# Optimization experiments

Hardware: AMD Instinct MI355X
Metric: run time of the kernel (lower is better)

The kernel has to match this reference:

```python
import jax, jax.numpy as jnp
import numpy as np
from jax import lax

EPS = 1e-5
S_CENTROIDS = 2048
K_NEIGH = 32


def _fps(xyz, S):
    """Farthest point sampling. xyz: (B,N,3) -> idx (B,S) int32."""
    B, N, _ = xyz.shape

    def body(carry, _):
        dist, farthest = carry  # (B,N), (B,)
        centroid = jnp.take_along_axis(xyz, farthest[:, None, None], axis=1)  # (B,1,3)
        d = jnp.sum((xyz - centroid) ** 2, axis=-1)  # (B,N)
        dist = jnp.minimum(dist, d)
        nxt = jnp.argmax(dist, axis=-1).astype(jnp.int32)
        return (dist, nxt), farthest

    init = (jnp.full((B, N), 1e10, xyz.dtype), jnp.zeros((B,), jnp.int32))
    _, idx = lax.scan(body, init, None, length=S)
    return idx.T  # (B,S)


def _knn(q, p, K):
    """q: (B,S,3) queries, p: (B,N,3) points -> idx (B,S,K) of K nearest."""
    d = (jnp.sum(q * q, -1)[:, :, None] + jnp.sum(p * p, -1)[:, None, :]
         - 2.0 * jnp.einsum('bsd,bnd->bsn', q, p))  # (B,S,N) sq dists
    _, idx = lax.top_k(-d, K)
    return idx


def _mlp_layer(x, w, g, b, m, v):
    # x: (B,S,K,Cin); 1x1 conv == channel matmul, then eval-mode BN, then ReLU
    x = jnp.einsum('bskc,oc->bsko', x, w)
    x = (x - m) * (g * lax.rsqrt(v + EPS)) + b
    return jax.nn.relu(x)


def setup_inputs() -> dict:
    key = jax.random.key(0)
    ks = jax.random.split(key, 8)
    B, N, D = 4, 8192, 64
    inp = {
        'xyz': jax.random.normal(ks[0], (B, N, 3), jnp.float32),
        'points': jax.random.normal(ks[1], (B, D, N), jnp.float32),
        'w0': jax.random.normal(ks[2], (64, 67), jnp.float32) * (1.0 / np.sqrt(67)),
        'g0': jnp.ones((64,), jnp.float32), 'b0': jnp.zeros((64,), jnp.float32),
        'm0': jnp.zeros((64,), jnp.float32), 'v0': jnp.ones((64,), jnp.float32),
        'w1': jax.random.normal(ks[3], (64, 64), jnp.float32) * (1.0 / np.sqrt(64)),
        'g1': jnp.ones((64,), jnp.float32), 'b1': jnp.zeros((64,), jnp.float32),
        'm1': jnp.zeros((64,), jnp.float32), 'v1': jnp.ones((64,), jnp.float32),
        'w2': jax.random.normal(ks[4], (128, 64), jnp.float32) * (1.0 / np.sqrt(64)),
        'g2': jnp.ones((128,), jnp.float32), 'b2': jnp.zeros((128,), jnp.float32),
        'm2': jnp.zeros((128,), jnp.float32), 'v2': jnp.ones((128,), jnp.float32),
    }
    return inp


def reference(xyz, points, w0, g0, b0, m0, v0, w1, g1, b1, m1, v1,
              w2, g2, b2, m2, v2):
    B, N, _ = xyz.shape
    S, K = S_CENTROIDS, K_NEIGH

    # FPS centroids (S < N path of the module)
    fps_idx = _fps(xyz, S)                                        # (B,S)
    new_xyz = jnp.take_along_axis(xyz, fps_idx[..., None], axis=1)  # (B,S,3)

    # KNN grouping
    idx = _knn(new_xyz, xyz, K)                                   # (B,S,K)
    grouped_xyz = jnp.take_along_axis(xyz[:, None], idx[..., None], axis=2)  # (B,S,K,3)
    grouped_xyz = grouped_xyz - new_xyz[:, :, None, :]

    # gather neighbor features: points (B,D,N) -> (B,N,D) -> (B,S,K,D)
    pts = jnp.transpose(points, (0, 2, 1))
    neigh = jnp.take_along_axis(pts[:, None], idx[..., None], axis=2)
    grouped = jnp.concatenate([grouped_xyz, neigh], axis=-1)      # (B,S,K,3+D)

    x = _mlp_layer(grouped, w0, g0, b0, m0, v0)
    x = _mlp_layer(x, w1, g1, b1, m1, v1)
    x = _mlp_layer(x, w2, g2, b2, m2, v2)                         # (B,S,K,128)

    new_points = jnp.transpose(jnp.max(x, axis=2), (0, 2, 1))     # (B,128,S)
    return new_xyz, new_points
```

## Files before the change

kernel.cpp:

```cpp
#include <hip/hip_runtime.h>
#include <cfloat>
#include <climits>

#define NPTS   8192
#define SCENT  2048
#define KNEIGH 32
#define BATCH  4
#define DFEAT  64
#define FPS_T  512
#define PPT    16
#define NW     8
#define CAP    64

#define DPPMAX(u, ctrl, rmask)                                                        \
    { unsigned _t = (unsigned)__builtin_amdgcn_update_dpp(0, (int)(u), (ctrl),        \
                                                          (rmask), 0xf, false);      \
      (u) = ((u) > _t) ? (u) : _t; }

__global__ __launch_bounds__(FPS_T, 1) void fps_kernel(const float* __restrict__ xyz,
                                                       float* __restrict__ new_xyz) {
    const int b = blockIdx.x, t = threadIdx.x;
    const int lane = t & 63, w = t >> 6;
    const float* X = xyz + (size_t)b * NPTS * 3;

    __shared__ float sx[NPTS], sy[NPTS], sz[NPTS];
    __shared__ float hx[SCENT], hy[SCENT], hz[SCENT];
    __shared__ uint2 slots[2][NW];
    __shared__ int   scand[CAP];
    __shared__ int   scnt;
    __shared__ double sdd[2][NW];
    __shared__ double sfv[NW];
    __shared__ int   sfo[NW];

    for (int p = t; p < NPTS; p += FPS_T) {
        sx[p] = X[3 * p + 0]; sy[p] = X[3 * p + 1]; sz[p] = X[3 * p + 2];
    }

    float px[PPT], py[PPT], pz[PPT], dist[PPT];
#pragma unroll
    for (int j = 0; j < PPT; ++j) {
        int p = t + FPS_T * j;
        px[j] = X[3 * p + 0]; py[j] = X[3 * p + 1]; pz[j] = X[3 * p + 2];
        dist[j] = 1e10f;
    }
    float cx = X[0], cy = X[1], cz = X[2];
    int buf = 0;
    __syncthreads();

#pragma unroll 1
    for (int s = 0; s < SCENT; ++s) {
        if (t == 0) { hx[s] = cx; hy[s] = cy; hz[s] = cz; }

        float ma = -1.f, mb = -1.f; int ia = 0, ib = 0;
#pragma unroll
        for (int j = 0; j < PPT; j += 2) {
            {
                float dx = px[j] - cx, dy = py[j] - cy, dz = pz[j] - cz;
                float d  = fmaf(dx, dx, fmaf(dy, dy, dz * dz));
                float nd = fminf(dist[j], d); dist[j] = nd;
                bool g = nd > ma; ma = g ? nd : ma; ia = g ? (t + FPS_T * j) : ia;
            }
            {
                float dx = px[j+1] - cx, dy = py[j+1] - cy, dz = pz[j+1] - cz;
                float d  = fmaf(dx, dx, fmaf(dy, dy, dz * dz));
                float nd = fminf(dist[j+1], d); dist[j+1] = nd;
                bool g = nd > mb; mb = g ? nd : mb; ib = g ? (t + FPS_T * (j+1)) : ib;
            }
        }
        bool gb = mb > ma;
        float m = gb ? mb : ma;
        int  mi = gb ? ib : ia;

        unsigned myU = __float_as_uint(m);
        unsigned u = myU;
        DPPMAX(u, 0x111, 0xf);
        DPPMAX(u, 0x112, 0xf);
        DPPMAX(u, 0x114, 0xf);
        DPPMAX(u, 0x118, 0xf);
        DPPMAX(u, 0x142, 0xa);
        DPPMAX(u, 0x143, 0xc);
        const unsigned wu = (unsigned)__builtin_amdgcn_readlane((int)u, 63);

        unsigned long long wb = __ballot(myU == wu);
        const int wl   = __ffsll(wb) - 1;
        const int widx = __builtin_amdgcn_readlane(mi, wl);
        const float thwf = __fmul_rn(__uint_as_float(wu), 0.999998f);
        int cnt = 0;
#pragma unroll
        for (int j = 0; j < PPT; ++j) cnt += (dist[j] >= thwf) ? 1 : 0;
        unsigned long long c1 = __ballot(cnt >= 1);
        unsigned long long c2 = __ballot(cnt >= 2);
        const unsigned tw = (c2 || __popcll(c1) >= 2) ? 1u : 0u;
        if (lane == 0)
            slots[buf][w] = make_uint2(wu, (unsigned)widx | (tw << 14));
        __syncthreads();

        uint2 sv[NW];
#pragma unroll
        for (int k = 0; k < NW; ++k) sv[k] = slots[buf][k];
        unsigned gu = sv[0].x;
#pragma unroll
        for (int k = 1; k < NW; ++k) gu = (sv[k].x > gu) ? sv[k].x : gu;
        const float gvf = __uint_as_float(gu);
        const float gthf = __fmul_rn(gvf, 0.999998f);
        const unsigned ugth = __float_as_uint(gthf);
        int nw = 0;
#pragma unroll
        for (int k = 0; k < NW; ++k) nw += (sv[k].x >= ugth) ? 1 : 0;
        unsigned meta = 0;
#pragma unroll
        for (int k = NW - 1; k >= 0; --k) if (sv[k].x == gu) meta = sv[k].y;
        const int wtie = (meta >> 14) & 1;
        int i1 = (int)(meta & 0x3fffu);

        if (nw >= 2 || wtie) {
            if (t == 0) scnt = 0;
            __syncthreads();
#pragma unroll
            for (int j = 0; j < PPT; ++j) {
                if (dist[j] >= gthf) {
                    int slot = atomicAdd(&scnt, 1);
                    if (slot < CAP) scand[slot] = t + FPS_T * j;
                }
            }
            __syncthreads();
            const int mm = scnt;
            if (mm <= CAP) {
                double bd = -1.0; int bi = INT_MAX;
#pragma unroll 1
                for (int k = 0; k < mm; ++k) {
                    const int pos = scand[k];
                    const double pxd = (double)sx[pos], pyd = (double)sy[pos],
                                 pzd = (double)sz[pos];
                    double dd = 1e10;
                    for (int i = t; i <= s; i += FPS_T) {
                        double ddx = __dsub_rn(pxd, (double)hx[i]);
                        double ddy = __dsub_rn(pyd, (double)hy[i]);
                        double ddz = __dsub_rn(pzd, (double)hz[i]);
                        double d = __dadd_rn(__dadd_rn(__dmul_rn(ddx, ddx), __dmul_rn(ddy, ddy)),
                                             __dmul_rn(ddz, ddz));
                        dd = fmin(dd, d);
                    }
#pragma unroll
                    for (int off = 32; off >= 1; off >>= 1)
                        dd = fmin(dd, __shfl_down(dd, off));
                    if (lane == 0) sdd[k & 1][w] = dd;
                    __syncthreads();
                    double ddm = sdd[k & 1][0];
#pragma unroll
                    for (int w2 = 1; w2 < NW; ++w2) ddm = fmin(ddm, sdd[k & 1][w2]);
                    if (ddm > bd || (ddm == bd && pos < bi)) { bd = ddm; bi = pos; }
                }
                i1 = bi;
            } else {
                double bv = -1.0; int bi = INT_MAX;
#pragma unroll 1
                for (int j = 0; j < PPT; ++j) {
                    const double pxd = (double)px[j], pyd = (double)py[j], pzd = (double)pz[j];
                    double dd = 1e10;
                    for (int i = 0; i <= s; ++i) {
                        double ddx = __dsub_rn(pxd, (double)hx[i]);
                        double ddy = __dsub_rn(pyd, (double)hy[i]);
                        double ddz = __dsub_rn(pzd, (double)hz[i]);
                        double d = __dadd_rn(__dadd_rn(__dmul_rn(ddx, ddx), __dmul_rn(ddy, ddy)),
                                             __dmul_rn(ddz, ddz));
                        dd = fmin(dd, d);
                    }
                    int pidx = t + FPS_T * j;
                    if (dd > bv || (dd == bv && pidx < bi)) { bv = dd; bi = pidx; }
                }
#pragma unroll
                for (int off = 32; off >= 1; off >>= 1) {
                    double ov = __shfl_down(bv, off);
                    int    oi = __shfl_down(bi, off);
                    if (ov > bv || (ov == bv && oi < bi)) { bv = ov; bi = oi; }
                }
                if (lane == 0) { sfv[w] = bv; sfo[w] = bi; }
                __syncthreads();
                bv = sfv[0]; bi = sfo[0];
#pragma unroll
                for (int w2 = 1; w2 < NW; ++w2) {
                    double ov = sfv[w2]; int oi = sfo[w2];
                    if (ov > bv || (ov == bv && oi < bi)) { bv = ov; bi = oi; }
                }
                i1 = bi;
            }
            __syncthreads();
        }
        cx = sx[i1]; cy = sy[i1]; cz = sz[i1];
        buf ^= 1;
    }
    __syncthreads();
    for (int i = t; i < SCENT; i += FPS_T) {
        float* o = new_xyz + (size_t)(b * SCENT + i) * 3;
        o[0] = hx[i]; o[1] = hy[i]; o[2] = hz[i];
    }
}

__global__ void transpose_kernel(const float* __restrict__ pts, float* __restrict__ out) {
    __shared__ float tile[32][33];
    const int b  = blockIdx.z;
    const int n0 = blockIdx.x * 32, d0 = blockIdx.y * 32;
    const int tx = threadIdx.x, ty = threadIdx.y;
#pragma unroll
    for (int i = 0; i < 4; ++i)
        tile[ty + 8 * i][tx] =
            pts[(size_t)b * DFEAT * NPTS + (size_t)(d0 + ty + 8 * i) * NPTS + n0 + tx];
    __syncthreads();
#pragma unroll
    for (int i = 0; i < 4; ++i)
        out[(size_t)b * NPTS * DFEAT + (size_t)(n0 + ty + 8 * i) * DFEAT + d0 + tx] =
            tile[tx][ty + 8 * i];
}

__global__ __launch_bounds__(256) void knn_kernel(const float* __restrict__ xyz,
                                                  const float* __restrict__ new_xyz,
                                                  int* __restrict__ knn_idx) {
    const int b    = blockIdx.y;
    const int wid  = threadIdx.x >> 6;
    const int lane = threadIdx.x & 63;
    const int qi   = blockIdx.x * 4 + wid;

    __shared__ float4 sp[2048];
    __shared__ double sp2[2048];

    const float* q = new_xyz + (size_t)(b * SCENT + qi) * 3;
    const double qx = (double)q[0], qy = (double)q[1], qz = (double)q[2];
    const double q2 = __dadd_rn(__dadd_rn(__dmul_rn(qx, qx), __dmul_rn(qy, qy)),
                                __dmul_rn(qz, qz));

    double ld   = DBL_MAX;
    int    li   = 0x7fffffff;
    double taud = DBL_MAX;
    int    taui = 0x7fffffff;

    const float* Xb = xyz + (size_t)b * NPTS * 3;
#pragma unroll 1
    for (int c = 0; c < 4; ++c) {
        __syncthreads();
#pragma unroll
        for (int r = 0; r < 8; ++r) {
            int pl = r * 256 + threadIdx.x;
            int p  = c * 2048 + pl;
            float x = Xb[3 * p + 0], y = Xb[3 * p + 1], z = Xb[3 * p + 2];
            sp[pl] = make_float4(x, y, z, 0.0f);
            double dx = (double)x, dy = (double)y, dz = (double)z;
            sp2[pl] = __dadd_rn(__dadd_rn(__dmul_rn(dx, dx), __dmul_rn(dy, dy)),
                                __dmul_rn(dz, dz));
        }
        __syncthreads();
#pragma unroll 1
        for (int i = 0; i < 32; ++i) {
            const int pl   = i * 64 + lane;
            const int pidx = c * 2048 + pl;
            float4 P = sp[pl];
            double px = (double)P.x, py = (double)P.y, pz = (double)P.z;
            double qp = __dadd_rn(__dadd_rn(__dmul_rn(qx, px), __dmul_rn(qy, py)),
                                  __dmul_rn(qz, pz));
            double d  = __dsub_rn(__dadd_rn(q2, sp2[pl]), __dmul_rn(2.0, qp));
            bool cand = (d < taud) || (d == taud && pidx < taui);
            unsigned long long m = __ballot(cand);
            while (m) {
                int sl = __ffsll((unsigned long long)m) - 1;
                m &= m - 1;
                double dv = __shfl(d, sl);
                int    iv = __shfl(pidx, sl);
                if (dv < taud || (dv == taud && iv < taui)) {
                    bool gt = (lane < 32) && (ld > dv || (ld == dv && li > iv));
                    unsigned long long gm = __ballot(gt);
                    double ud = __shfl_up(ld, 1);
                    int    ui = __shfl_up(li, 1);
                    if (gt) { ld = ud; li = ui; }
                    bool first = gt && ((lane == 0) || !((gm >> (lane - 1)) & 1ull));
                    if (first) { ld = dv; li = iv; }
                    taud = __shfl(ld, 31);
                    taui = __shfl(li, 31);
                }
            }
        }
    }
    if (lane < 32) knn_idx[(size_t)(b * SCENT + qi) * KNEIGH + lane] = li;
}

__global__ __launch_bounds__(256) void mlp_kernel(
    const float* __restrict__ xyz, const float* __restrict__ new_xyz,
    const float* __restrict__ ptsT, const int* __restrict__ knn_idx,
    const float* __restrict__ w0, const float* __restrict__ g0,
    const float* __restrict__ b0, const float* __restrict__ m0,
    const float* __restrict__ v0, const float* __restrict__ w1,
    const float* __restrict__ g1, const float* __restrict__ b1,
    const float* __restrict__ m1, const float* __restrict__ v1,
    const float* __restrict__ w2, const float* __restrict__ g2,
    const float* __restrict__ b2, const float* __restrict__ m2,
    const float* __restrict__ v2, float* __restrict__ out_points) {

    __shared__ float regA[8192];
    __shared__ float regB[4096];
    __shared__ float prm[512];

    const int t = threadIdx.x;
    if (t < 64) {
        float a0v = g0[t] / sqrtf(v0[t] + 1e-5f);
        prm[t]       = a0v;
        prm[64 + t]  = b0[t] - m0[t] * a0v;
        float a1v = g1[t] / sqrtf(v1[t] + 1e-5f);
        prm[128 + t] = a1v;
        prm[192 + t] = b1[t] - m1[t] * a1v;
    } else if (t < 192) {
        int o = t - 64;
        float a2v = g2[o] / sqrtf(v2[o] + 1e-5f);
        prm[256 + o] = a2v;
        prm[384 + o] = b2[o] - m2[o] * a2v;
    }
    for (int idx = t; idx < 64 * 68; idx += 256) {
        int o = idx / 68, i = idx - o * 68;
        float v;
        if (i < 64)      v = w0[o * 67 + 3 + i];
        else if (i < 67) v = w0[o * 67 + (i - 64)];
        else             v = 0.0f;
        regA[idx] = v;
    }
    for (int idx = t; idx < 64 * 64; idx += 256) regB[idx] = w1[idx];
    __syncthreads();

    const int gid = blockIdx.x * 256 + t;
    const int sl  = gid >> 5;
    const int s   = sl & (SCENT - 1);
    const int b   = sl >> 11;
    const int nidx = knn_idx[gid];

    const float* q  = new_xyz + (size_t)(b * SCENT + s) * 3;
    const float* P3 = xyz + (size_t)(b * NPTS + nidx) * 3;
    const float dx = P3[0] - q[0], dy = P3[1] - q[1], dz = P3[2] - q[2];

    const float4* F = (const float4*)(ptsT + ((size_t)b * NPTS + nidx) * 64);
    float4 xv[17];
#pragma unroll
    for (int i = 0; i < 16; ++i) xv[i] = F[i];
    xv[16] = make_float4(dx, dy, dz, 0.0f);

    float h0[64];
    const float4* W0 = (const float4*)regA;
#pragma unroll
    for (int o = 0; o < 64; ++o) {
        float acc = 0.f;
#pragma unroll
        for (int i = 0; i < 17; ++i) {
            float4 w = W0[o * 17 + i];
            acc = fmaf(xv[i].x, w.x, acc);
            acc = fmaf(xv[i].y, w.y, acc);
            acc = fmaf(xv[i].z, w.z, acc);
            acc = fmaf(xv[i].w, w.w, acc);
        }
        h0[o] = fmaxf(fmaf(acc, prm[o], prm[64 + o]), 0.f);
    }
    __syncthreads();
    for (int idx = t; idx < 128 * 64; idx += 256) regA[idx] = w2[idx];
    __syncthreads();

    float h1[64];
    const float4* W1 = (const float4*)regB;
#pragma unroll
    for (int o = 0; o < 64; ++o) {
        float acc = 0.f;
#pragma unroll
        for (int i = 0; i < 16; ++i) {
            float4 w = W1[o * 16 + i];
            acc = fmaf(h0[4 * i + 0], w.x, acc);
            acc = fmaf(h0[4 * i + 1], w.y, acc);
            acc = fmaf(h0[4 * i + 2], w.z, acc);
            acc = fmaf(h0[4 * i + 3], w.w, acc);
        }
        h1[o] = fmaxf(fmaf(acc, prm[128 + o], prm[192 + o]), 0.f);
    }

    const float4* W2 = (const float4*)regA;
    float* outp = out_points + (size_t)b * 128 * SCENT + s;
    const int lane = t & 63;
#pragma unroll 1
    for (int o = 0; o < 128; ++o) {
        float acc = 0.f;
#pragma unroll
        for (int i = 0; i < 16; ++i) {
            float4 w = W2[o * 16 + i];
            acc = fmaf(h1[4 * i + 0], w.x, acc);
            acc = fmaf(h1[4 * i + 1], w.y, acc);
            acc = fmaf(h1[4 * i + 2], w.z, acc);
            acc = fmaf(h1[4 * i + 3], w.w, acc);
        }
        float y = fmaxf(fmaf(acc, prm[256 + o], prm[384 + o]), 0.f);
#pragma unroll
        for (int off = 16; off >= 1; off >>= 1) y = fmaxf(y, __shfl_xor(y, off));
        if ((lane & 31) == 0) outp[(size_t)o * SCENT] = y;
    }
}

extern "C" void kernel_launch(void* const* d_in, const int* in_sizes, int n_in,
                              void* d_out, int out_size, void* d_ws, size_t ws_size,
                              hipStream_t stream) {
    const float* xyz    = (const float*)d_in[0];
    const float* points = (const float*)d_in[1];
    const float* w0 = (const float*)d_in[2];
    const float* g0 = (const float*)d_in[3];
    const float* b0 = (const float*)d_in[4];
    const float* m0 = (const float*)d_in[5];
    const float* v0 = (const float*)d_in[6];
    const float* w1 = (const float*)d_in[7];
    const float* g1 = (const float*)d_in[8];
    const float* b1 = (const float*)d_in[9];
    const float* m1 = (const float*)d_in[10];
    const float* v1 = (const float*)d_in[11];
    const float* w2 = (const float*)d_in[12];
    const float* g2 = (const float*)d_in[13];
    const float* b2 = (const float*)d_in[14];
    const float* m2 = (const float*)d_in[15];
    const float* v2 = (const float*)d_in[16];

    float* out_xyz    = (float*)d_out;
    float* out_points = (float*)d_out + (size_t)BATCH * SCENT * 3;

    char* ws = (char*)d_ws;
    int*   knn_idx = (int*)(ws + 32768);
    float* ptsT    = (float*)(ws + 32768 + (size_t)BATCH * SCENT * KNEIGH * 4);

    fps_kernel<<<BATCH, FPS_T, 0, stream>>>(xyz, out_xyz);
    transpose_kernel<<<dim3(NPTS / 32, DFEAT / 32, BATCH), dim3(32, 8), 0, stream>>>(points, ptsT);
    knn_kernel<<<dim3(SCENT / 4, BATCH), 256, 0, stream>>>(xyz, out_xyz, knn_idx);
    mlp_kernel<<<(BATCH * SCENT * KNEIGH) / 256, 256, 0, stream>>>(
        xyz, out_xyz, ptsT, knn_idx,
        w0, g0, b0, m0, v0, w1, g1, b1, m1, v1, w2, g2, b2, m2, v2, out_points);
}
```

Measured before the change: 2.714 ms.

## Vectorize FPS distance update with packed float2 and publish winner coordinates directly

Rewrites the FPS inner loop to use two-wide float vectors, which lets the compiler emit packed FP32 math. Per-thread argmax index tracking is dropped, and only the winning wave later recovers the winner's coordinates and checks for ties. Those coordinates go through shared memory, so the shared-memory copies of all point coordinates are removed. The cost is a second block barrier per iteration, which lengthens the serial critical path.

Result: no change. 2.761 ms (+1.7%).

```diff
diff --git a/kernel.cpp b/kernel.cpp
--- a/kernel.cpp
+++ b/kernel.cpp
@@ -8,9 +8,11 @@
 #define BATCH  4
 #define DFEAT  64
 #define FPS_T  512
-#define PPT    16
+#define NV     8
 #define NW     8
 #define CAP    64
+
+typedef float v2f __attribute__((ext_vector_type(2)));
 
 #define DPPMAX(u, ctrl, rmask)                                                        \
     { unsigned _t = (unsigned)__builtin_amdgcn_update_dpp(0, (int)(u), (ctrl),        \
@@ -23,25 +25,25 @@
     const int lane = t & 63, w = t >> 6;
     const float* X = xyz + (size_t)b * NPTS * 3;
 
-    __shared__ float sx[NPTS], sy[NPTS], sz[NPTS];
     __shared__ float hx[SCENT], hy[SCENT], hz[SCENT];
-    __shared__ uint2 slots[2][NW];
+    __shared__ __align__(16) unsigned slot1[2][NW];
+    __shared__ __align__(16) float4 pub[2];
     __shared__ int   scand[CAP];
+    __shared__ float scandX[CAP], scandY[CAP], scandZ[CAP];
     __shared__ int   scnt;
     __shared__ double sdd[2][NW];
     __shared__ double sfv[NW];
-    __shared__ int   sfo[NW];
-
-    for (int p = t; p < NPTS; p += FPS_T) {
-        sx[p] = X[3 * p + 0]; sy[p] = X[3 * p + 1]; sz[p] = X[3 * p + 2];
-    }
-
-    float px[PPT], py[PPT], pz[PPT], dist[PPT];
-#pragma unroll
-    for (int j = 0; j < PPT; ++j) {
-        int p = t + FPS_T * j;
-        px[j] = X[3 * p + 0]; py[j] = X[3 * p + 1]; pz[j] = X[3 * p + 2];
-        dist[j] = 1e10f;
+    __shared__ int    sfo[NW];
+    __shared__ float  sfc[3];
+
+    v2f px2[NV], py2[NV], pz2[NV], dist2[NV];
+#pragma unroll
+    for (int j = 0; j < NV; ++j) {
+        int pA = t + FPS_T * j, pB = t + FPS_T * (j + NV);
+        px2[j] = (v2f){X[3 * pA + 0], X[3 * pB + 0]};
+        py2[j] = (v2f){X[3 * pA + 1], X[3 * pB + 1]};
+        pz2[j] = (v2f){X[3 * pA + 2], X[3 * pB + 2]};
+        dist2[j] = (v2f){1e10f, 1e10f};
     }
     float cx = X[0], cy = X[1], cz = X[2];
     int buf = 0;
@@ -51,25 +53,20 @@
     for (int s = 0; s < SCENT; ++s) {
         if (t == 0) { hx[s] = cx; hy[s] = cy; hz[s] = cz; }
 
-        float ma = -1.f, mb = -1.f; int ia = 0, ib = 0;
-#pragma unroll
-        for (int j = 0; j < PPT; j += 2) {
-            {
-                float dx = px[j] - cx, dy = py[j] - cy, dz = pz[j] - cz;
-                float d  = fmaf(dx, dx, fmaf(dy, dy, dz * dz));
-                float nd = fminf(dist[j], d); dist[j] = nd;
-                bool g = nd > ma; ma = g ? nd : ma; ia = g ? (t + FPS_T * j) : ia;
-            }
-            {
-                float dx = px[j+1] - cx, dy = py[j+1] - cy, dz = pz[j+1] - cz;
-                float d  = fmaf(dx, dx, fmaf(dy, dy, dz * dz));
-                float nd = fminf(dist[j+1], d); dist[j+1] = nd;
-                bool g = nd > mb; mb = g ? nd : mb; ib = g ? (t + FPS_T * (j+1)) : ib;
-            }
-        }
-        bool gb = mb > ma;
-        float m = gb ? mb : ma;
-        int  mi = gb ? ib : ia;
+        const v2f cxx = {cx, cx}, cyy = {cy, cy}, czz = {cz, cz};
+        v2f m2 = {-1.f, -1.f};
+#pragma unroll
+        for (int j = 0; j < NV; ++j) {
+            v2f dx = px2[j] - cxx;
+            v2f dy = py2[j] - cyy;
+            v2f dz = pz2[j] - czz;
+            v2f d  = __builtin_elementwise_fma(dx, dx,
+                     __builtin_elementwise_fma(dy, dy, dz * dz));
+            v2f nd = __builtin_elementwise_min(dist2[j], d);
+            dist2[j] = nd;
+            m2 = __builtin_elementwise_max(m2, nd);
+        }
+        const float m = fmaxf(m2.x, m2.y);
 
         unsigned myU = __float_as_uint(m);
         unsigned u = myU;
@@ -80,58 +77,86 @@
         DPPMAX(u, 0x142, 0xa);
         DPPMAX(u, 0x143, 0xc);
         const unsigned wu = (unsigned)__builtin_amdgcn_readlane((int)u, 63);
-
-        unsigned long long wb = __ballot(myU == wu);
-        const int wl   = __ffsll(wb) - 1;
-        const int widx = __builtin_amdgcn_readlane(mi, wl);
-        const float thwf = __fmul_rn(__uint_as_float(wu), 0.999998f);
-        int cnt = 0;
-#pragma unroll
-        for (int j = 0; j < PPT; ++j) cnt += (dist[j] >= thwf) ? 1 : 0;
-        unsigned long long c1 = __ballot(cnt >= 1);
-        unsigned long long c2 = __ballot(cnt >= 2);
-        const unsigned tw = (c2 || __popcll(c1) >= 2) ? 1u : 0u;
-        if (lane == 0)
-            slots[buf][w] = make_uint2(wu, (unsigned)widx | (tw << 14));
+        if (lane == 0) slot1[buf][w] = wu;
         __syncthreads();
 
-        uint2 sv[NW];
-#pragma unroll
-        for (int k = 0; k < NW; ++k) sv[k] = slots[buf][k];
-        unsigned gu = sv[0].x;
-#pragma unroll
-        for (int k = 1; k < NW; ++k) gu = (sv[k].x > gu) ? sv[k].x : gu;
-        const float gvf = __uint_as_float(gu);
-        const float gthf = __fmul_rn(gvf, 0.999998f);
+        unsigned sv[NW];
+        {
+            const uint4* sp = (const uint4*)&slot1[buf][0];
+            uint4 a = sp[0], c = sp[1];
+            sv[0] = a.x; sv[1] = a.y; sv[2] = a.z; sv[3] = a.w;
+            sv[4] = c.x; sv[5] = c.y; sv[6] = c.z; sv[7] = c.w;
+        }
+        unsigned gu = sv[0];
+#pragma unroll
+        for (int k = 1; k < NW; ++k) gu = (sv[k] > gu) ? sv[k] : gu;
+        const float gv   = __uint_as_float(gu);
+        const float gthf = __fmul_rn(gv, 0.999998f);
         const unsigned ugth = __float_as_uint(gthf);
-        int nw = 0;
-#pragma unroll
-        for (int k = 0; k < NW; ++k) nw += (sv[k].x >= ugth) ? 1 : 0;
-        unsigned meta = 0;
-#pragma unroll
-        for (int k = NW - 1; k >= 0; --k) if (sv[k].x == gu) meta = sv[k].y;
-        const int wtie = (meta >> 14) & 1;
-        int i1 = (int)(meta & 0x3fffu);
-
-        if (nw >= 2 || wtie) {
+        int nw = 0, k0 = 0;
+#pragma unroll
+        for (int k = NW - 1; k >= 0; --k) {
+            nw += (sv[k] >= ugth) ? 1 : 0;
+            k0 = (sv[k] == gu) ? k : k0;
+        }
+
+        if (w == k0) {
+            int cnt = 0;
+            float wxc = 0.f, wyc = 0.f, wzc = 0.f;
+#pragma unroll
+            for (int j = 0; j < NV; ++j) {
+                bool cA = dist2[j].x >= gthf, cB = dist2[j].y >= gthf;
+                cnt += (cA ? 1 : 0) + (cB ? 1 : 0);
+                bool eA = dist2[j].x == gv, eB = dist2[j].y == gv;
+                wxc = eA ? px2[j].x : wxc; wxc = eB ? px2[j].y : wxc;
+                wyc = eA ? py2[j].x : wyc; wyc = eB ? py2[j].y : wyc;
+                wzc = eA ? pz2[j].x : wzc; wzc = eB ? pz2[j].y : wzc;
+            }
+            unsigned long long wb = __ballot(m == gv);
+            const int wl = __ffsll(wb) - 1;
+            int xi = __builtin_amdgcn_readlane((int)__float_as_uint(wxc), wl);
+            int yi = __builtin_amdgcn_readlane((int)__float_as_uint(wyc), wl);
+            int zi = __builtin_amdgcn_readlane((int)__float_as_uint(wzc), wl);
+            unsigned long long c2 = __ballot(cnt >= 2);
+            unsigned long long c1 = __ballot(cnt >= 1);
+            unsigned tie = (c2 || __popcll(c1) >= 2) ? 1u : 0u;
+            if (lane == 0)
+                pub[buf] = make_float4(__uint_as_float(xi), __uint_as_float(yi),
+                                       __uint_as_float(zi), __uint_as_float(tie));
+        }
+        __syncthreads();
+        const float4 P = pub[buf];
+        const unsigned tieg = __float_as_uint(P.w);
+
+        if (nw >= 2 || tieg) {
             if (t == 0) scnt = 0;
             __syncthreads();
 #pragma unroll
-            for (int j = 0; j < PPT; ++j) {
-                if (dist[j] >= gthf) {
+            for (int j = 0; j < NV; ++j) {
+                if (dist2[j].x >= gthf) {
                     int slot = atomicAdd(&scnt, 1);
-                    if (slot < CAP) scand[slot] = t + FPS_T * j;
+                    if (slot < CAP) {
+                        scand[slot] = t + FPS_T * j;
+                        scandX[slot] = px2[j].x; scandY[slot] = py2[j].x; scandZ[slot] = pz2[j].x;
+                    }
+                }
+                if (dist2[j].y >= gthf) {
+                    int slot = atomicAdd(&scnt, 1);
+                    if (slot < CAP) {
+                        scand[slot] = t + FPS_T * (j + NV);
+                        scandX[slot] = px2[j].y; scandY[slot] = py2[j].y; scandZ[slot] = pz2[j].y;
+                    }
                 }
             }
             __syncthreads();
             const int mm = scnt;
             if (mm <= CAP) {
-                double bd = -1.0; int bi = INT_MAX;
+                double bd = -1.0; int bi = INT_MAX; float bx = cx, by = cy, bz = cz;
 #pragma unroll 1
                 for (int k = 0; k < mm; ++k) {
                     const int pos = scand[k];
-                    const double pxd = (double)sx[pos], pyd = (double)sy[pos],
-                                 pzd = (double)sz[pos];
+                    const double pxd = (double)scandX[k], pyd = (double)scandY[k],
+                                 pzd = (double)scandZ[k];
                     double dd = 1e10;
                     for (int i = t; i <= s; i += FPS_T) {
                         double ddx = __dsub_rn(pxd, (double)hx[i]);
@@ -149,14 +174,21 @@
                     double ddm = sdd[k & 1][0];
 #pragma unroll
                     for (int w2 = 1; w2 < NW; ++w2) ddm = fmin(ddm, sdd[k & 1][w2]);
-                    if (ddm > bd || (ddm == bd && pos < bi)) { bd = ddm; bi = pos; }
-                }
-                i1 = bi;
+                    if (ddm > bd || (ddm == bd && pos < bi)) {
+                        bd = ddm; bi = pos;
+                        bx = scandX[k]; by = scandY[k]; bz = scandZ[k];
+                    }
+                }
+                cx = bx; cy = by; cz = bz;
             } else {
                 double bv = -1.0; int bi = INT_MAX;
 #pragma unroll 1
-                for (int j = 0; j < PPT; ++j) {
-                    const double pxd = (double)px[j], pyd = (double)py[j], pzd = (double)pz[j];
+                for (int j = 0; j < 2 * NV; ++j) {
+                    const int jj = j & (NV - 1);
+                    const bool hiHalf = j >= NV;
+                    const double pxd = (double)(hiHalf ? px2[jj].y : px2[jj].x);
+                    const double pyd = (double)(hiHalf ? py2[jj].y : py2[jj].x);
+                    const double pzd = (double)(hiHalf ? pz2[jj].y : pz2[jj].x);
                     double dd = 1e10;
                     for (int i = 0; i <= s; ++i) {
                         double ddx = __dsub_rn(pxd, (double)hx[i]);
@@ -183,11 +215,27 @@
                     double ov = sfv[w2]; int oi = sfo[w2];
                     if (ov > bv || (ov == bv && oi < bi)) { bv = ov; bi = oi; }
                 }
-                i1 = bi;
+                if ((bi & (FPS_T - 1)) == t) {
+                    float ox = 0.f, oy = 0.f, oz = 0.f;
+#pragma unroll
+                    for (int j = 0; j < 2 * NV; ++j) {
+                        const int jj = j & (NV - 1);
+                        bool c = (bi == t + FPS_T * j);
+                        bool hiHalf = j >= NV;
+                        float vx = hiHalf ? px2[jj].y : px2[jj].x;
+                        float vy = hiHalf ? py2[jj].y : py2[jj].x;
+                        float vz = hiHalf ? pz2[jj].y : pz2[jj].x;
+                        ox = c ? vx : ox; oy = c ? vy : oy; oz = c ? vz : oz;
+                    }
+                    sfc[0] = ox; sfc[1] = oy; sfc[2] = oz;
+                }
+                __syncthreads();
+                cx = sfc[0]; cy = sfc[1]; cz = sfc[2];
             }
             __syncthreads();
-        }
-        cx = sx[i1]; cy = sy[i1]; cz = sz[i1];
+        } else {
+            cx = P.x; cy = P.y; cz = P.z;
+        }
         buf ^= 1;
     }
     __syncthreads();
```
